# Kernel tuning notes

Hardware: AMD Instinct MI355X
Metric: run time of the kernel (lower is better)

The kernel has to match this reference:

```python
import jax, jax.numpy as jnp
import numpy as np

N_FRAG = 1_000_000
CELL_N = 1000
GENE_N = 500
N_GENES = 5000
H = 100   # hidden dims
E = 100   # embedding dims


def setup_inputs() -> dict:
    key = jax.random.key(0)
    ks = jax.random.split(key, 16)
    coords = jax.random.randint(ks[0], (N_FRAG, 2), 0, 1000, dtype=jnp.int64 if jax.config.jax_enable_x64 else jnp.int32)
    cxg_ix = jnp.sort(jax.random.randint(ks[1], (N_FRAG,), 0, CELL_N * GENE_N))
    gene_ix = jax.random.randint(ks[2], (GENE_N,), 0, N_GENES)
    stdv_in = 1.0 / np.sqrt(2)
    stdv_h = 1.0 / np.sqrt(H)
    u = lambda k, shape, s: jax.random.uniform(k, shape, jnp.float32, -s, s)
    W0 = u(ks[3], (2, H), stdv_in); b0 = u(ks[4], (H,), stdv_in)
    W1 = u(ks[5], (H, H), stdv_h); b1 = u(ks[6], (H,), stdv_h)
    W2 = u(ks[7], (H, H), stdv_h); b2 = u(ks[8], (H,), stdv_h)
    W3 = u(ks[9], (H, E), stdv_h); b3 = u(ks[10], (E,), stdv_h)
    weight1 = u(ks[11], (N_GENES, E), stdv_h / 100.0)  # torch init: stdv/100
    bias1 = jax.random.normal(ks[12], (N_GENES,), jnp.float32)  # mean gene expression
    return {
        "fragment_coordinates": coords,
        "fragment_cellxgene_ix": cxg_ix,
        "cell_n": CELL_N,
        "gene_n": GENE_N,
        "gene_ix": gene_ix,
        "W0": W0, "b0": b0, "W1": W1, "b1": b1,
        "W2": W2, "b2": b2, "W3": W3, "b3": b3,
        "weight1": weight1, "bias1": bias1,
    }


def reference(fragment_coordinates, fragment_cellxgene_ix, cell_n, gene_n, gene_ix,
              W0, b0, W1, b1, W2, b2, W3, b3, weight1, bias1):
    # FragmentEmbedder: 4-layer MLP on scaled coordinates
    x = fragment_coordinates.astype(jnp.float32) / 1000.0          # [F, 2]
    h = jax.nn.relu(x @ W0 + b0)
    h = jax.nn.relu(h @ W1 + b1)
    h = jax.nn.relu(h @ W2 + b2)
    emb = h @ W3 + b3                                              # [F, E]
    # EmbeddingGenePooler: segment-sum into cell x gene bins
    pooled = jax.ops.segment_sum(emb, fragment_cellxgene_ix,
                                 num_segments=cell_n * gene_n)     # [C*G, E]
    cg = pooled.reshape(cell_n, gene_n, -1)                        # [C, G, E]
    # EmbeddingToExpression: gene-specific weighted sum + bias
    out = jnp.einsum('cge,ge->cg', cg, weight1[gene_ix]) + bias1[gene_ix]
    return out
```

## Files before the change

kernel.cpp:

```cpp
#include <hip/hip_runtime.h>
#include <hip/hip_bf16.h>

typedef __attribute__((ext_vector_type(4))) short s16x4;
typedef __attribute__((ext_vector_type(4))) float f32x4;
typedef __attribute__((ext_vector_type(8))) unsigned short u16x8;
typedef __attribute__((ext_vector_type(8))) __bf16 bf16x8;

#define GENE_N     500
#define WG_STRIDE  112
#define WG_OFF_BYTES 81920
#define OFF_B_BYTES 3584
#define OFF_C_BYTES 68096
#define NFRAG_TOTAL 91

__device__ __forceinline__ unsigned short f2bf(float x){
  __hip_bfloat16 h = __float2bfloat16(x);
  return *reinterpret_cast<unsigned short*>(&h);
}

__device__ __forceinline__ f32x4 mfma16(s16x4 a, s16x4 b, f32x4 c){
  return __builtin_amdgcn_mfma_f32_16x16x16bf16_1k(a, b, c, 0, 0, 0);
}

__device__ __forceinline__ f32x4 mfma32(bf16x8 a, bf16x8 b, f32x4 c){
  return __builtin_amdgcn_mfma_f32_16x16x32_bf16(a, b, c, 0, 0, 0);
}

__global__ void init_out(const int* __restrict__ gene_ix,
                         const float* __restrict__ bias1,
                         float* __restrict__ out, int n){
  int t = blockIdx.x*blockDim.x + threadIdx.x;
  if (t < n) out[t] = bias1[gene_ix[t % GENE_N]];
}

__global__ void prep_weights(const float* __restrict__ W0, const float* __restrict__ b0,
                             const float* __restrict__ W1, const float* __restrict__ b1,
                             const float* __restrict__ W2, const float* __restrict__ b2,
                             const float* __restrict__ W3, const float* __restrict__ b3,
                             unsigned short* __restrict__ wsW){
  int t = blockIdx.x*blockDim.x + threadIdx.x;
  if (t >= NFRAG_TOTAL*64) return;
  int fr = t >> 6, lane = t & 63;
  int grp = lane >> 4, row = lane & 15;

  if (fr < 7){
    int up = fr*16 + row;
    unsigned short* dst = wsW + (fr*64 + lane)*4;
    #pragma unroll
    for (int i = 0; i < 4; ++i){
      int k = grp*4 + i;
      float val = 0.f;
      if (up < 100){
        if (k < 2)       val = W0[k*100 + up];
        else if (k == 2) val = b0[up];
      }
      dst[i] = f2bf(val);
    }
  } else if (fr < 70){
    int fb = fr - 7;
    int L = fb/21, m = (fb%21)/3, q = fb%3;
    const float* W = (L==0)?W1:(L==1)?W2:W3;
    const float* B = (L==0)?b1:(L==1)?b2:b3;
    int up = m*16 + row;
    unsigned short* dst = wsW + OFF_B_BYTES/2 + (fb*64 + lane)*8;
    #pragma unroll
    for (int i = 0; i < 8; ++i){
      int k = 32*q + ((i < 4) ? (grp*4 + i) : (16 + grp*4 + (i-4)));
      float val = 0.f;
      if (up < 100){
        if (k < 100)       val = W[k*100 + up];
        else if (k == 100) val = B[up];
      }
      dst[i] = f2bf(val);
    }
  } else {
    int fc = fr - 70;
    int L = fc/7, m = fc%7;
    const float* W = (L==0)?W1:(L==1)?W2:W3;
    const float* B = (L==0)?b1:(L==1)?b2:b3;
    int up = m*16 + row;
    unsigned short* dst = wsW + OFF_C_BYTES/2 + (fc*64 + lane)*4;
    #pragma unroll
    for (int i = 0; i < 4; ++i){
      int k = 96 + grp*4 + i;
      float val = 0.f;
      if (up < 100){
        if (k < 100)       val = W[k*100 + up];
        else if (k == 100) val = B[up];
      }
      dst[i] = f2bf(val);
    }
  }
}

__global__ void prep_wg(const int* __restrict__ gene_ix,
                        const float* __restrict__ weight1,
                        float* __restrict__ wg){
  int t = blockIdx.x*blockDim.x + threadIdx.x;
  if (t >= GENE_N*WG_STRIDE) return;
  int g = t / WG_STRIDE, e = t % WG_STRIDE;
  wg[t] = (e < 100) ? weight1[gene_ix[g]*100 + e] : 0.f;
}


__device__ __forceinline__ unsigned fbits(float x){ return __builtin_bit_cast(unsigned, x); }

__device__ __forceinline__ void pack_relu2(const f32x4* __restrict__ acc,
                                           unsigned* __restrict__ pl,
                                           unsigned* __restrict__ ph, bool selb){
  #pragma unroll
  for (int m = 0; m < 7; ++m){
    unsigned u0 = fbits(fmaxf(acc[m][0], 0.f)) + 0x8000u;
    unsigned u1 = fbits(fmaxf(acc[m][1], 0.f)) + 0x8000u;
    unsigned u2 = fbits(fmaxf(acc[m][2], 0.f)) + 0x8000u;
    unsigned u3 = fbits(fmaxf(acc[m][3], 0.f)) + 0x8000u;
    unsigned lo = __builtin_amdgcn_perm(u1, u0, 0x07060302u);
    unsigned hi = __builtin_amdgcn_perm(u3, u2, 0x07060302u);
    if (m == 6) lo = selb ? ((lo & 0xFFFF0000u) | 0x3F80u) : lo;
    pl[m] = lo; ph[m] = hi;
  }
}

__device__ __forceinline__ bf16x8 catB(unsigned a0, unsigned a1, unsigned b0, unsigned b1){
  uint4 u; u.x = a0; u.y = a1; u.z = b0; u.w = b1;
  return __builtin_bit_cast(bf16x8, u);
}

__device__ __forceinline__ void hidden_layer(const bf16x8* __restrict__ Wd,
                                             const s16x4* __restrict__ Wt,
                                             const unsigned* __restrict__ pl,
                                             const unsigned* __restrict__ ph,
                                             f32x4* __restrict__ acc){
  const f32x4 zero = {0.f,0.f,0.f,0.f};
  bf16x8 B0 = catB(pl[0], ph[0], pl[1], ph[1]);
  bf16x8 B1 = catB(pl[2], ph[2], pl[3], ph[3]);
  bf16x8 B2 = catB(pl[4], ph[4], pl[5], ph[5]);
  uint2 t6; t6.x = pl[6]; t6.y = ph[6];
  s16x4 b6 = __builtin_bit_cast(s16x4, t6);
  #pragma unroll
  for (int m = 0; m < 7; ++m){
    f32x4 a = mfma32(Wd[3*m  ], B0, zero);
    a       = mfma32(Wd[3*m+1], B1, a);
    a       = mfma32(Wd[3*m+2], B2, a);
    a       = mfma16(Wt[m],     b6, a);
    acc[m] = a;
  }
}

__device__ __forceinline__ void epi_store(const f32x4* __restrict__ acc,
                                          const float* __restrict__ wg,
                                          int grp, int lane, int f, int nfrag,
                                          int cxgv, float* __restrict__ out){
  int gbin = cxgv % GENE_N;
  const float* wrow = wg + gbin*WG_STRIDE + grp*4;
  float s = 0.f;
  #pragma unroll
  for (int m = 0; m < 7; ++m){
    float4 w = *(const float4*)(wrow + m*16);
    s += acc[m][0]*w.x + acc[m][1]*w.y + acc[m][2]*w.z + acc[m][3]*w.w;
  }
  s += __shfl_xor(s, 16);
  s += __shfl_xor(s, 32);
  if (lane < 16 && f < nfrag) atomicAdd(out + cxgv, s);
}

__device__ __forceinline__ s16x4 build_bx(int2 cd){
  s16x4 v;
  v[0] = (short)f2bf((float)cd.x * 1e-3f);
  v[1] = (short)f2bf((float)cd.y * 1e-3f);
  v[2] = (short)0x3F80;
  v[3] = 0;
  return v;
}

__global__ __launch_bounds__(64, 1)
void frag_mlp_pool(const int* __restrict__ coords, const int* __restrict__ cxg,
                   const unsigned short* __restrict__ wsW,
                   const float* __restrict__ wg,
                   float* __restrict__ out, int nfrag, int ntiles){
  const int lane = threadIdx.x & 63;
  const int grp = lane >> 4, row = lane & 15;
  const bool selb = (grp == 1);

  const s16x4* wfA = (const s16x4*)wsW;
  const u16x8* wfB = (const u16x8*)(wsW + OFF_B_BYTES/2);
  const s16x4* wfC = (const s16x4*)(wsW + OFF_C_BYTES/2);

  s16x4 A0[7];
  bf16x8 W1d[21], W2d[21], W3d[21];
  s16x4 W1t[7], W2t[7], W3t[7];
  #pragma unroll
  for (int i = 0; i < 7;  ++i) A0[i] = wfA[i*64 + lane];
  #pragma unroll
  for (int i = 0; i < 21; ++i) W1d[i] = __builtin_bit_cast(bf16x8, wfB[(i     )*64 + lane]);
  #pragma unroll
  for (int i = 0; i < 21; ++i) W2d[i] = __builtin_bit_cast(bf16x8, wfB[(21 + i)*64 + lane]);
  #pragma unroll
  for (int i = 0; i < 21; ++i) W3d[i] = __builtin_bit_cast(bf16x8, wfB[(42 + i)*64 + lane]);
  #pragma unroll
  for (int i = 0; i < 7;  ++i) W1t[i] = wfC[(i     )*64 + lane];
  #pragma unroll
  for (int i = 0; i < 7;  ++i) W2t[i] = wfC[( 7 + i)*64 + lane];
  #pragma unroll
  for (int i = 0; i < 7;  ++i) W3t[i] = wfC[(14 + i)*64 + lane];

  const f32x4 zero = {0.f,0.f,0.f,0.f};
  const int npairs = (ntiles + 1) >> 1;
  const int lastf = nfrag - 1;

  int p0 = blockIdx.x;
  int fA = p0*32 + row, fB = p0*32 + 16 + row;
  int cA = (fA < nfrag) ? fA : lastf;
  int cB = (fB < nfrag) ? fB : lastf;
  int2 cdA = ((const int2*)coords)[cA];
  int2 cdB = ((const int2*)coords)[cB];
  int  xgA = cxg[cA];
  int  xgB = cxg[cB];

  for (int p = p0; p < npairs; p += gridDim.x){
    int f0 = p*32 + row, f1 = p*32 + 16 + row;
    int2 cd0 = cdA, cd1 = cdB;
    int  xg0 = xgA, xg1 = xgB;

    int pn = p + gridDim.x;
    int fAn = pn*32 + row, fBn = pn*32 + 16 + row;
    int cAn = (fAn < nfrag) ? fAn : lastf;
    int cBn = (fBn < nfrag) ? fBn : lastf;
    cdA = ((const int2*)coords)[cAn];
    cdB = ((const int2*)coords)[cBn];
    xgA = cxg[cAn];
    xgB = cxg[cBn];

    s16x4 bx0 = build_bx(cd0);
    s16x4 bx1 = build_bx(cd1);
    f32x4 acc0[7], acc1[7];
    #pragma unroll
    for (int m = 0; m < 7; ++m) acc0[m] = mfma16(A0[m], bx0, zero);
    #pragma unroll
    for (int m = 0; m < 7; ++m) acc1[m] = mfma16(A0[m], bx1, zero);

    unsigned pl0[7], ph0[7], pl1[7], ph1[7];
    pack_relu2(acc0, pl0, ph0, selb);
    hidden_layer(W1d, W1t, pl0, ph0, acc0);   pack_relu2(acc1, pl1, ph1, selb);
    hidden_layer(W1d, W1t, pl1, ph1, acc1);   pack_relu2(acc0, pl0, ph0, selb);
    hidden_layer(W2d, W2t, pl0, ph0, acc0);   pack_relu2(acc1, pl1, ph1, selb);
    hidden_layer(W2d, W2t, pl1, ph1, acc1);   pack_relu2(acc0, pl0, ph0, selb);
    hidden_layer(W3d, W3t, pl0, ph0, acc0);   pack_relu2(acc1, pl1, ph1, selb);
    hidden_layer(W3d, W3t, pl1, ph1, acc1);

    epi_store(acc0, wg, grp, lane, f0, nfrag, xg0, out);
    epi_store(acc1, wg, grp, lane, f1, nfrag, xg1, out);
  }
}

extern "C" void kernel_launch(void* const* d_in, const int* in_sizes, int n_in,
                              void* d_out, int out_size, void* d_ws, size_t ws_size,
                              hipStream_t stream){
  const int* coords  = (const int*)d_in[0];
  const int* cxg     = (const int*)d_in[1];
  const int* gene_ix = (const int*)d_in[4];
  const float* W0 = (const float*)d_in[5];
  const float* b0 = (const float*)d_in[6];
  const float* W1 = (const float*)d_in[7];
  const float* b1 = (const float*)d_in[8];
  const float* W2 = (const float*)d_in[9];
  const float* b2 = (const float*)d_in[10];
  const float* W3 = (const float*)d_in[11];
  const float* b3 = (const float*)d_in[12];
  const float* weight1 = (const float*)d_in[13];
  const float* bias1   = (const float*)d_in[14];

  int nfrag  = in_sizes[1];
  int ntiles = (nfrag + 15) / 16;

  unsigned short* wsW = (unsigned short*)d_ws;
  float* wg = (float*)((char*)d_ws + WG_OFF_BYTES);
  float* out = (float*)d_out;

  hipLaunchKernelGGL(init_out, dim3((out_size + 255)/256), dim3(256), 0, stream,
                     gene_ix, bias1, out, out_size);
  hipLaunchKernelGGL(prep_weights, dim3((NFRAG_TOTAL*64 + 255)/256), dim3(256), 0, stream,
                     W0, b0, W1, b1, W2, b2, W3, b3, wsW);
  hipLaunchKernelGGL(prep_wg, dim3((GENE_N*WG_STRIDE + 255)/256), dim3(256), 0, stream,
                     gene_ix, weight1, wg);
  hipLaunchKernelGGL(frag_mlp_pool, dim3(1024), dim3(64), 0, stream,
                     coords, cxg, wsW, wg, out, nfrag, ntiles);
}
```

Measured before the change: 172.0 us.

## Stage hidden-layer weights in LDS and run four waves per block

Moves the dense hidden-layer weight fragments from per-lane registers into shared memory, loaded once per 256-thread block. Each hidden layer now processes both fragment tiles together and reads the weights from LDS. The bias is dropped from the B fragments and folded into the tail MFMA, which now runs first. The aim is to cut register pressure so more waves fit per CU and hide latency, at the cost of LDS reads inside the inner loop and an initial copy plus barrier.

```diff
diff --git a/kernel.cpp b/kernel.cpp
--- a/kernel.cpp
+++ b/kernel.cpp
@@ -12,6 +12,7 @@
 #define OFF_B_BYTES 3584
 #define OFF_C_BYTES 68096
 #define NFRAG_TOTAL 91
+#define LDS_BYTES   63488
 
 __device__ __forceinline__ unsigned short f2bf(float x){
   __hip_bfloat16 h = __float2bfloat16(x);
@@ -21,7 +22,6 @@
 __device__ __forceinline__ f32x4 mfma16(s16x4 a, s16x4 b, f32x4 c){
   return __builtin_amdgcn_mfma_f32_16x16x16bf16_1k(a, b, c, 0, 0, 0);
 }
-
 __device__ __forceinline__ f32x4 mfma32(bf16x8 a, bf16x8 b, f32x4 c){
   return __builtin_amdgcn_mfma_f32_16x16x32_bf16(a, b, c, 0, 0, 0);
 }
@@ -60,17 +60,13 @@
     int fb = fr - 7;
     int L = fb/21, m = (fb%21)/3, q = fb%3;
     const float* W = (L==0)?W1:(L==1)?W2:W3;
-    const float* B = (L==0)?b1:(L==1)?b2:b3;
     int up = m*16 + row;
     unsigned short* dst = wsW + OFF_B_BYTES/2 + (fb*64 + lane)*8;
     #pragma unroll
     for (int i = 0; i < 8; ++i){
       int k = 32*q + ((i < 4) ? (grp*4 + i) : (16 + grp*4 + (i-4)));
       float val = 0.f;
-      if (up < 100){
-        if (k < 100)       val = W[k*100 + up];
-        else if (k == 100) val = B[up];
-      }
+      if (up < 100 && k < 100) val = W[k*100 + up];
       dst[i] = f2bf(val);
     }
   } else {
@@ -126,24 +122,42 @@
   return __builtin_bit_cast(bf16x8, u);
 }
 
-__device__ __forceinline__ void hidden_layer(const bf16x8* __restrict__ Wd,
-                                             const s16x4* __restrict__ Wt,
-                                             const unsigned* __restrict__ pl,
-                                             const unsigned* __restrict__ ph,
-                                             f32x4* __restrict__ acc){
+__device__ __forceinline__ bf16x8 ldsFrag(const unsigned char* lds, int fb, int lane){
+  return *(const bf16x8*)(lds + fb*1024 + lane*16);
+}
+
+template<int L>
+__device__ __forceinline__ void hidden_lds(const unsigned char* __restrict__ lds, int lane,
+                                           const s16x4* __restrict__ Wt, bf16x8 WB62,
+                                           const unsigned* __restrict__ pl0, const unsigned* __restrict__ ph0,
+                                           const unsigned* __restrict__ pl1, const unsigned* __restrict__ ph1,
+                                           f32x4* __restrict__ acc0, f32x4* __restrict__ acc1){
   const f32x4 zero = {0.f,0.f,0.f,0.f};
-  bf16x8 B0 = catB(pl[0], ph[0], pl[1], ph[1]);
-  bf16x8 B1 = catB(pl[2], ph[2], pl[3], ph[3]);
-  bf16x8 B2 = catB(pl[4], ph[4], pl[5], ph[5]);
-  uint2 t6; t6.x = pl[6]; t6.y = ph[6];
-  s16x4 b6 = __builtin_bit_cast(s16x4, t6);
+  bf16x8 B00 = catB(pl0[0], ph0[0], pl0[1], ph0[1]);
+  bf16x8 B01 = catB(pl0[2], ph0[2], pl0[3], ph0[3]);
+  bf16x8 B02 = catB(pl0[4], ph0[4], pl0[5], ph0[5]);
+  uint2 t0; t0.x = pl0[6]; t0.y = ph0[6];
+  s16x4 b60 = __builtin_bit_cast(s16x4, t0);
+  bf16x8 B10 = catB(pl1[0], ph1[0], pl1[1], ph1[1]);
+  bf16x8 B11 = catB(pl1[2], ph1[2], pl1[3], ph1[3]);
+  bf16x8 B12 = catB(pl1[4], ph1[4], pl1[5], ph1[5]);
+  uint2 t1; t1.x = pl1[6]; t1.y = ph1[6];
+  s16x4 b61 = __builtin_bit_cast(s16x4, t1);
   #pragma unroll
   for (int m = 0; m < 7; ++m){
-    f32x4 a = mfma32(Wd[3*m  ], B0, zero);
-    a       = mfma32(Wd[3*m+1], B1, a);
-    a       = mfma32(Wd[3*m+2], B2, a);
-    a       = mfma16(Wt[m],     b6, a);
-    acc[m] = a;
+    const int fb = L*21 + m*3;
+    bf16x8 w0 = ldsFrag(lds, fb,   lane);
+    bf16x8 w1 = ldsFrag(lds, fb+1, lane);
+    bf16x8 w2 = (fb+2 == 62) ? WB62 : ldsFrag(lds, fb+2, lane);
+    f32x4 a0 = mfma16(Wt[L*7+m], b60, zero);
+    a0 = mfma32(w0, B00, a0);
+    a0 = mfma32(w1, B01, a0);
+    a0 = mfma32(w2, B02, a0);
+    f32x4 a1 = mfma16(Wt[L*7+m], b61, zero);
+    a1 = mfma32(w0, B10, a1);
+    a1 = mfma32(w1, B11, a1);
+    a1 = mfma32(w2, B12, a1);
+    acc0[m] = a0; acc1[m] = a1;
   }
 }
 
@@ -173,12 +187,22 @@
   return v;
 }
 
-__global__ __launch_bounds__(64, 1)
+__global__ __launch_bounds__(256, 2)
 void frag_mlp_pool(const int* __restrict__ coords, const int* __restrict__ cxg,
                    const unsigned short* __restrict__ wsW,
                    const float* __restrict__ wg,
                    float* __restrict__ out, int nfrag, int ntiles){
+  __shared__ __align__(16) unsigned char ldsW[LDS_BYTES];
+
+  {
+    const uint4* src = (const uint4*)((const unsigned char*)wsW + OFF_B_BYTES);
+    uint4* dst = (uint4*)ldsW;
+    for (int t = threadIdx.x; t < LDS_BYTES/16; t += 256) dst[t] = src[t];
+  }
+  __syncthreads();
+
   const int lane = threadIdx.x & 63;
+  const int wid  = threadIdx.x >> 6;
   const int grp = lane >> 4, row = lane & 15;
   const bool selb = (grp == 1);
 
@@ -186,30 +210,20 @@
   const u16x8* wfB = (const u16x8*)(wsW + OFF_B_BYTES/2);
   const s16x4* wfC = (const s16x4*)(wsW + OFF_C_BYTES/2);
 
-  s16x4 A0[7];
-  bf16x8 W1d[21], W2d[21], W3d[21];
-  s16x4 W1t[7], W2t[7], W3t[7];
+  s16x4 A0[7], Wt[21];
   #pragma unroll
   for (int i = 0; i < 7;  ++i) A0[i] = wfA[i*64 + lane];
   #pragma unroll
-  for (int i = 0; i < 21; ++i) W1d[i] = __builtin_bit_cast(bf16x8, wfB[(i     )*64 + lane]);
-  #pragma unroll
-  for (int i = 0; i < 21; ++i) W2d[i] = __builtin_bit_cast(bf16x8, wfB[(21 + i)*64 + lane]);
-  #pragma unroll
-  for (int i = 0; i < 21; ++i) W3d[i] = __builtin_bit_cast(bf16x8, wfB[(42 + i)*64 + lane]);
-  #pragma unroll
-  for (int i = 0; i < 7;  ++i) W1t[i] = wfC[(i     )*64 + lane];
-  #pragma unroll
-  for (int i = 0; i < 7;  ++i) W2t[i] = wfC[( 7 + i)*64 + lane];
-  #pragma unroll
-  for (int i = 0; i < 7;  ++i) W3t[i] = wfC[(14 + i)*64 + lane];
+  for (int i = 0; i < 21; ++i) Wt[i] = wfC[i*64 + lane];
+  bf16x8 WB62 = __builtin_bit_cast(bf16x8, wfB[62*64 + lane]);
 
   const f32x4 zero = {0.f,0.f,0.f,0.f};
   const int npairs = (ntiles + 1) >> 1;
   const int lastf = nfrag - 1;
-
-  int p0 = blockIdx.x;
-  int fA = p0*32 + row, fB = p0*32 + 16 + row;
+  const int gw = blockIdx.x*4 + wid;
+  const int nw = gridDim.x*4;
+
+  int fA = gw*32 + row, fB = gw*32 + 16 + row;
   int cA = (fA < nfrag) ? fA : lastf;
   int cB = (fB < nfrag) ? fB : lastf;
   int2 cdA = ((const int2*)coords)[cA];
@@ -217,12 +231,12 @@
   int  xgA = cxg[cA];
   int  xgB = cxg[cB];
 
-  for (int p = p0; p < npairs; p += gridDim.x){
+  for (int p = gw; p < npairs; p += nw){
     int f0 = p*32 + row, f1 = p*32 + 16 + row;
     int2 cd0 = cdA, cd1 = cdB;
     int  xg0 = xgA, xg1 = xgB;
 
-    int pn = p + gridDim.x;
+    int pn = p + nw;
     int fAn = pn*32 + row, fBn = pn*32 + 16 + row;
     int cAn = (fAn < nfrag) ? fAn : lastf;
     int cBn = (fBn < nfrag) ? fBn : lastf;
@@ -241,12 +255,14 @@
 
     unsigned pl0[7], ph0[7], pl1[7], ph1[7];
     pack_relu2(acc0, pl0, ph0, selb);
-    hidden_layer(W1d, W1t, pl0, ph0, acc0);   pack_relu2(acc1, pl1, ph1, selb);
-    hidden_layer(W1d, W1t, pl1, ph1, acc1);   pack_relu2(acc0, pl0, ph0, selb);
-    hidden_layer(W2d, W2t, pl0, ph0, acc0);   pack_relu2(acc1, pl1, ph1, selb);
-    hidden_layer(W2d, W2t, pl1, ph1, acc1);   pack_relu2(acc0, pl0, ph0, selb);
-    hidden_layer(W3d, W3t, pl0, ph0, acc0);   pack_relu2(acc1, pl1, ph1, selb);
-    hidden_layer(W3d, W3t, pl1, ph1, acc1);
+    pack_relu2(acc1, pl1, ph1, selb);
+    hidden_lds<0>(ldsW, lane, Wt, WB62, pl0, ph0, pl1, ph1, acc0, acc1);
+    pack_relu2(acc0, pl0, ph0, selb);
+    pack_relu2(acc1, pl1, ph1, selb);
+    hidden_lds<1>(ldsW, lane, Wt, WB62, pl0, ph0, pl1, ph1, acc0, acc1);
+    pack_relu2(acc0, pl0, ph0, selb);
+    pack_relu2(acc1, pl1, ph1, selb);
+    hidden_lds<2>(ldsW, lane, Wt, WB62, pl0, ph0, pl1, ph1, acc0, acc1);
 
     epi_store(acc0, wg, grp, lane, f0, nfrag, xg0, out);
     epi_store(acc1, wg, grp, lane, f1, nfrag, xg1, out);
@@ -283,6 +299,6 @@
                      W0, b0, W1, b1, W2, b2, W3, b3, wsW);
   hipLaunchKernelGGL(prep_wg, dim3((GENE_N*WG_STRIDE + 255)/256), dim3(256), 0, stream,
                      gene_ix, weight1, wg);
-  hipLaunchKernelGGL(frag_mlp_pool, dim3(1024), dim3(64), 0, stream,
+  hipLaunchKernelGGL(frag_mlp_pool, dim3(512), dim3(256), 0, stream,
                      coords, cxg, wsW, wg, out, nfrag, ntiles);
 }
```

Measured after the change: 333.7 us. 94.0% more time.
